# Performance work log

Hardware: AMD Instinct MI355X
Metric: run time of the kernel (lower is better)

The kernel has to match this reference:

```python
import jax, jax.numpy as jnp
import numpy as np

S, B, SC = 2048, 1024, 256 * 16  # shops, bundles, styles*colors


def setup_inputs() -> dict:
    key = jax.random.key(0)
    k1, k2, k3, k4 = jax.random.split(key, 4)
    return {
        "proba": jax.random.normal(k1, (S * B,), dtype=jnp.float32),
        "cur_inven": jax.random.uniform(k2, (S, SC), dtype=jnp.float32),
        "bun_sc": jax.random.uniform(k3, (B, SC), dtype=jnp.float32),
        "avail_bundle": jax.random.uniform(k4, (B,), dtype=jnp.float32),
        "alloc_bundle": jnp.zeros((B,), dtype=jnp.float32),
    }


def reference(proba, cur_inven, bun_sc, avail_bundle, alloc_bundle):
    # proba[i] with i = shop*B + bundle  ->  [S, B]
    p = proba.reshape(S, B)
    # constraint_multiplier: 0.01 if over-availability (p>0) or over-negative-alloc (p<0)
    over_avail = (avail_bundle[None, :] - p < 0.0) & (p > 0.0)
    over_alloc = (alloc_bundle[None, :] + p < 0.0) & (p < 0.0)
    cm = jnp.where(over_avail | over_alloc, jnp.float32(0.01), jnp.float32(1.0))
    # next_inven[s, sc] = cur[s, sc] + sum_b bun_sc[b, sc] * p[s, b] * cm[s, b]
    next_inven = cur_inven + jnp.einsum('sb,bc->sc', p * cm, bun_sc)
    return next_inven.reshape(1, -1)
```

## Files before the change

kernel.cpp:

```cpp
#include <hip/hip_runtime.h>

#define S_DIM  2048
#define B_DIM  1024
#define SC_DIM 4096

#define BM 128
#define BN 128
#define BK 64

typedef __bf16 bf16x8 __attribute__((ext_vector_type(8)));
typedef float  f32x4  __attribute__((ext_vector_type(4)));
typedef unsigned short u16x4 __attribute__((ext_vector_type(4)));
typedef unsigned short u16x8 __attribute__((ext_vector_type(8)));

__device__ __forceinline__ unsigned short f2bf(float f) {
    unsigned int u = __builtin_bit_cast(unsigned int, f);
    return (unsigned short)((u + 0x7FFFu + ((u >> 16) & 1u)) >> 16);
}

__device__ __forceinline__ void gld_lds16(const void* g, void* l) {
    __builtin_amdgcn_global_load_lds(
        (const __attribute__((address_space(1))) unsigned int*)g,
        (__attribute__((address_space(3))) unsigned int*)l, 16, 0, 0);
}

__global__ __launch_bounds__(256)
void prepack_ab(const float* __restrict__ proba,
                const float* __restrict__ avail,
                const float* __restrict__ alloc,
                const float* __restrict__ bsc,
                unsigned short* __restrict__ wsA,
                unsigned short* __restrict__ wsB)
{
    __shared__ float lds[64][129];
    const int t = threadIdx.x;

    if (blockIdx.x < 1024) {
        int c = blockIdx.x * 256 + t;
        int n = c >> 7;
        int G = c & 127;
        int k = G * 8;

        f32x4 p0 = *(const f32x4*)&proba[(size_t)n * B_DIM + k];
        f32x4 p1 = *(const f32x4*)&proba[(size_t)n * B_DIM + k + 4];
        f32x4 av0 = *(const f32x4*)&avail[k];
        f32x4 av1 = *(const f32x4*)&avail[k + 4];
        f32x4 al0 = *(const f32x4*)&alloc[k];
        f32x4 al1 = *(const f32x4*)&alloc[k + 4];

        u16x8 w;
        #pragma unroll
        for (int i = 0; i < 4; ++i) {
            float pv = p0[i];
            bool oa = (av0[i] - pv < 0.f) && (pv > 0.f);
            bool ob = (al0[i] + pv < 0.f) && (pv < 0.f);
            w[i] = f2bf(pv * ((oa || ob) ? 0.01f : 1.0f));
        }
        #pragma unroll
        for (int i = 0; i < 4; ++i) {
            float pv = p1[i];
            bool oa = (av1[i] - pv < 0.f) && (pv > 0.f);
            bool ob = (al1[i] + pv < 0.f) && (pv < 0.f);
            w[4 + i] = f2bf(pv * ((oa || ob) ? 0.01f : 1.0f));
        }
        int Gs = (G & ~7) | ((G & 7) ^ (n & 7));
        *(u16x8*)&wsA[(size_t)n * B_DIM + Gs * 8] = w;
    } else {
        int b2 = blockIdx.x - 1024;
        const int bn0 = (b2 & 31) * 128;
        const int k0  = (b2 >> 5) * 64;

        #pragma unroll
        for (int p = 0; p < 8; ++p) {
            int kl = (t >> 5) + p * 8;
            int cl = (t & 31) * 4;
            f32x4 v = *(const f32x4*)&bsc[(size_t)(k0 + kl) * SC_DIM + bn0 + cl];
            lds[kl][cl]     = v[0];
            lds[kl][cl + 1] = v[1];
            lds[kl][cl + 2] = v[2];
            lds[kl][cl + 3] = v[3];
        }
        __syncthreads();

        #pragma unroll
        for (int p = 0; p < 4; ++p) {
            int g = t & 7;
            int n = (t >> 3) + p * 32;
            u16x8 w;
            #pragma unroll
            for (int i = 0; i < 8; ++i)
                w[i] = f2bf(lds[g * 8 + i][n]);
            int gs = g ^ (n & 7);
            *(u16x8*)&wsB[(size_t)(bn0 + n) * B_DIM + k0 + gs * 8] = w;
        }
    }
}

__global__ __launch_bounds__(256, 2)
void gemm_pk(const unsigned short* __restrict__ wsA,
             const unsigned short* __restrict__ wsB,
             const float* __restrict__ cur,
             float* __restrict__ out)
{
    __shared__ __align__(16) unsigned short sA[BM * BK];
    __shared__ __align__(16) unsigned short sB[BN * BK];

    const int tid  = threadIdx.x;
    const int lane = tid & 63;
    const int wid  = tid >> 6;
    const int wm   = wid >> 1;
    const int wn   = wid & 1;
    const int l16  = lane & 15;
    const int lg   = lane >> 4;

    const int bid    = blockIdx.x;
    const int x      = bid & 7;
    const int l      = bid >> 3;
    const int n_tile = x * 4 + (l & 3);
    const int m_tile = l >> 2;
    const int bm0    = m_tile * BM;
    const int bn0    = n_tile * BN;

    const int crow = tid >> 3;
    const int cg   = tid & 7;

    f32x4 acc[4][4];
    #pragma unroll
    for (int i = 0; i < 4; ++i)
        #pragma unroll
        for (int j = 0; j < 4; ++j)
            acc[i][j] = {0.f, 0.f, 0.f, 0.f};

    auto stage = [&](int k0) {
        #pragma unroll
        for (int is = 0; is < 4; ++is)
            gld_lds16(wsA + (size_t)(bm0 + is * 32 + crow) * B_DIM + k0 + cg * 8,
                      &sA[(is * 256 + tid) * 8]);
        #pragma unroll
        for (int is = 0; is < 4; ++is)
            gld_lds16(wsB + (size_t)(bn0 + is * 32 + crow) * B_DIM + k0 + cg * 8,
                      &sB[(is * 256 + tid) * 8]);
    };

    const int NT = B_DIM / BK;
    stage(0);

    for (int t = 0; t < NT; ++t) {
        __syncthreads();

        bf16x8 afr[2][4], bfr[2][4];
        #pragma unroll
        for (int kk = 0; kk < 2; ++kk) {
            #pragma unroll
            for (int mf = 0; mf < 4; ++mf) {
                int r = wm * 64 + mf * 16 + l16;
                afr[kk][mf] = *(const bf16x8*)&sA[r * BK + (((kk * 4 + lg) ^ (r & 7)) * 8)];
            }
            #pragma unroll
            for (int nf = 0; nf < 4; ++nf) {
                int r = wn * 64 + nf * 16 + l16;
                bfr[kk][nf] = *(const bf16x8*)&sB[r * BK + (((kk * 4 + lg) ^ (r & 7)) * 8)];
            }
        }
        __syncthreads();

        if (t < NT - 1)
            stage((t + 1) * BK);
        __builtin_amdgcn_sched_barrier(0);

        #pragma unroll
        for (int kk = 0; kk < 2; ++kk)
            #pragma unroll
            for (int mf = 0; mf < 4; ++mf)
                #pragma unroll
                for (int nf = 0; nf < 4; ++nf)
                    acc[mf][nf] = __builtin_amdgcn_mfma_f32_16x16x32_bf16(
                        afr[kk][mf], bfr[kk][nf], acc[mf][nf], 0, 0, 0);
    }

    #pragma unroll
    for (int mf = 0; mf < 4; ++mf)
        #pragma unroll
        for (int j = 0; j < 4; ++j)
            #pragma unroll
            for (int nf = 0; nf < 4; ++nf) {
                int row = bm0 + wm * 64 + mf * 16 + lg * 4 + j;
                int col = bn0 + wn * 64 + nf * 16 + l16;
                size_t idx = (size_t)row * SC_DIM + col;
                out[idx] = cur[idx] + acc[mf][nf][j];
            }
}

#define FBM 128
#define FBN 128
#define LDK 72
__global__ __launch_bounds__(256, 2)
void opt_gemm_fused(const float* __restrict__ proba,
                    const float* __restrict__ cur,
                    const float* __restrict__ bsc,
                    const float* __restrict__ avail,
                    const float* __restrict__ alloc,
                    float* __restrict__ out)
{
    __shared__ __align__(16) unsigned short sA[FBM * LDK];
    __shared__ __align__(16) unsigned short sB[FBN * LDK];
    const int tid = threadIdx.x;
    const int lane = tid & 63;
    const int wid = tid >> 6;
    const int wm = wid >> 1, wn = wid & 1;
    const int bm0 = blockIdx.y * FBM, bn0 = blockIdx.x * FBN;
    const int af4 = tid & 15, ar0 = tid >> 4;
    const int bnn = tid & 127, bkh = tid >> 7;
    const int l16 = lane & 15, lg = lane >> 4;

    f32x4 acc[4][4];
    #pragma unroll
    for (int i = 0; i < 4; ++i)
        #pragma unroll
        for (int j = 0; j < 4; ++j) acc[i][j] = {0.f, 0.f, 0.f, 0.f};

    for (int k0 = 0; k0 < B_DIM; k0 += BK) {
        f32x4 av = *(const f32x4*)&avail[k0 + af4 * 4];
        f32x4 al = *(const f32x4*)&alloc[k0 + af4 * 4];
        #pragma unroll
        for (int pass = 0; pass < 8; ++pass) {
            int r = ar0 + pass * 16;
            f32x4 p = *(const f32x4*)&proba[(size_t)(bm0 + r) * B_DIM + k0 + af4 * 4];
            u16x4 w;
            #pragma unroll
            for (int i = 0; i < 4; ++i) {
                float pv = p[i];
                bool oa = (av[i] - pv < 0.f) && (pv > 0.f);
                bool ob = (al[i] + pv < 0.f) && (pv < 0.f);
                w[i] = f2bf(pv * ((oa || ob) ? 0.01f : 1.0f));
            }
            *(u16x4*)&sA[r * LDK + af4 * 4] = w;
        }
        #pragma unroll
        for (int g = 0; g < 4; ++g) {
            u16x8 w;
            #pragma unroll
            for (int i = 0; i < 8; ++i) {
                int kk = bkh * 32 + g * 8 + i;
                w[i] = f2bf(bsc[(size_t)(k0 + kk) * SC_DIM + bn0 + bnn]);
            }
            *(u16x8*)&sB[bnn * LDK + bkh * 32 + g * 8] = w;
        }
        __syncthreads();
        #pragma unroll
        for (int kk = 0; kk < 2; ++kk) {
            bf16x8 afr[4], bfr[4];
            #pragma unroll
            for (int mf = 0; mf < 4; ++mf)
                afr[mf] = *(const bf16x8*)&sA[(wm * 64 + mf * 16 + l16) * LDK + kk * 32 + lg * 8];
            #pragma unroll
            for (int nf = 0; nf < 4; ++nf)
                bfr[nf] = *(const bf16x8*)&sB[(wn * 64 + nf * 16 + l16) * LDK + kk * 32 + lg * 8];
            #pragma unroll
            for (int mf = 0; mf < 4; ++mf)
                #pragma unroll
                for (int nf = 0; nf < 4; ++nf)
                    acc[mf][nf] = __builtin_amdgcn_mfma_f32_16x16x32_bf16(
                        afr[mf], bfr[nf], acc[mf][nf], 0, 0, 0);
        }
        __syncthreads();
    }
    #pragma unroll
    for (int mf = 0; mf < 4; ++mf)
        #pragma unroll
        for (int j = 0; j < 4; ++j) {
            int row = bm0 + wm * 64 + mf * 16 + lg * 4 + j;
            #pragma unroll
            for (int nf = 0; nf < 4; ++nf) {
                int col = bn0 + wn * 64 + nf * 16 + l16;
                size_t idx = (size_t)row * SC_DIM + col;
                out[idx] = cur[idx] + acc[mf][nf][j];
            }
        }
}

extern "C" void kernel_launch(void* const* d_in, const int* in_sizes, int n_in,
                              void* d_out, int out_size, void* d_ws, size_t ws_size,
                              hipStream_t stream) {
    const float* proba = (const float*)d_in[0];
    const float* cur   = (const float*)d_in[1];
    const float* bsc   = (const float*)d_in[2];
    const float* avail = (const float*)d_in[3];
    const float* alloc = (const float*)d_in[4];
    float* out = (float*)d_out;

    const size_t wsA_bytes = (size_t)S_DIM * B_DIM * 2;
    const size_t wsB_bytes = (size_t)SC_DIM * B_DIM * 2;

    if (ws_size >= wsA_bytes + wsB_bytes) {
        unsigned short* wsA = (unsigned short*)d_ws;
        unsigned short* wsB = (unsigned short*)((char*)d_ws + wsA_bytes);

        prepack_ab<<<dim3(1024 + 512), 256, 0, stream>>>(proba, avail, alloc, bsc, wsA, wsB);
        gemm_pk<<<dim3((S_DIM / BM) * (SC_DIM / BN)), 256, 0, stream>>>(wsA, wsB, cur, out);
    } else {
        opt_gemm_fused<<<dim3(SC_DIM / FBN, S_DIM / FBM), 256, 0, stream>>>(
            proba, cur, bsc, avail, alloc, out);
    }
}
```

Before: 36.25 us.

## Prepack A in MFMA fragment order and load it directly into registers

The prepack kernel now writes the masked bf16 A operand in per-lane MFMA fragment order, so the GEMM loads A fragments straight from global memory into registers and no longer stages A through LDS. A is register double-buffered across iterations (aP/aQ) with prefetch of the next tile, while B still goes through LDS. This removes LDS traffic and shared memory for A, at the cost of more registers and uncached global loads per wave, since A rows are reread by each wn wave.

```diff
diff --git a/kernel.cpp b/kernel.cpp
--- a/kernel.cpp
+++ b/kernel.cpp
@@ -37,12 +37,17 @@
 
     if (blockIdx.x < 1024) {
         int c = blockIdx.x * 256 + t;
-        int n = c >> 7;
-        int G = c & 127;
-        int k = G * 8;
-
-        f32x4 p0 = *(const f32x4*)&proba[(size_t)n * B_DIM + k];
-        f32x4 p1 = *(const f32x4*)&proba[(size_t)n * B_DIM + k + 4];
+        int lane = c & 63;
+        int fragslot = c >> 6;
+        int mg = fragslot >> 5;
+        int kb = fragslot & 31;
+        int l16 = lane & 15;
+        int lg  = lane >> 4;
+        int row = mg * 16 + l16;
+        int k   = kb * 32 + lg * 8;
+
+        f32x4 p0 = *(const f32x4*)&proba[(size_t)row * B_DIM + k];
+        f32x4 p1 = *(const f32x4*)&proba[(size_t)row * B_DIM + k + 4];
         f32x4 av0 = *(const f32x4*)&avail[k];
         f32x4 av1 = *(const f32x4*)&avail[k + 4];
         f32x4 al0 = *(const f32x4*)&alloc[k];
@@ -63,8 +68,7 @@
             bool ob = (al1[i] + pv < 0.f) && (pv < 0.f);
             w[4 + i] = f2bf(pv * ((oa || ob) ? 0.01f : 1.0f));
         }
-        int Gs = (G & ~7) | ((G & 7) ^ (n & 7));
-        *(u16x8*)&wsA[(size_t)n * B_DIM + Gs * 8] = w;
+        *(u16x8*)&wsA[(size_t)c * 8] = w;
     } else {
         int b2 = blockIdx.x - 1024;
         const int bn0 = (b2 & 31) * 128;
@@ -102,7 +106,6 @@
              const float* __restrict__ cur,
              float* __restrict__ out)
 {
-    __shared__ __align__(16) unsigned short sA[BM * BK];
     __shared__ __align__(16) unsigned short sB[BN * BK];
 
     const int tid  = threadIdx.x;
@@ -124,6 +127,8 @@
     const int crow = tid >> 3;
     const int cg   = tid & 7;
 
+    const int mgBase = (bm0 >> 4) + wm * 4;
+
     f32x4 acc[4][4];
     #pragma unroll
     for (int i = 0; i < 4; ++i)
@@ -131,41 +136,45 @@
         for (int j = 0; j < 4; ++j)
             acc[i][j] = {0.f, 0.f, 0.f, 0.f};
 
-    auto stage = [&](int k0) {
-        #pragma unroll
-        for (int is = 0; is < 4; ++is)
-            gld_lds16(wsA + (size_t)(bm0 + is * 32 + crow) * B_DIM + k0 + cg * 8,
-                      &sA[(is * 256 + tid) * 8]);
+    auto stageB = [&](int k0) {
         #pragma unroll
         for (int is = 0; is < 4; ++is)
             gld_lds16(wsB + (size_t)(bn0 + is * 32 + crow) * B_DIM + k0 + cg * 8,
                       &sB[(is * 256 + tid) * 8]);
     };
 
-    const int NT = B_DIM / BK;
-    stage(0);
-
-    for (int t = 0; t < NT; ++t) {
-        __syncthreads();
-
-        bf16x8 afr[2][4], bfr[2][4];
-        #pragma unroll
-        for (int kk = 0; kk < 2; ++kk) {
-            #pragma unroll
-            for (int mf = 0; mf < 4; ++mf) {
-                int r = wm * 64 + mf * 16 + l16;
-                afr[kk][mf] = *(const bf16x8*)&sA[r * BK + (((kk * 4 + lg) ^ (r & 7)) * 8)];
-            }
+    const unsigned short* aBase = wsA + ((size_t)mgBase * 32 * 64 + lane) * 8;
+
+    auto loadA = [&](int t, bf16x8 (&dst)[2][4]) {
+        #pragma unroll
+        for (int kk = 0; kk < 2; ++kk)
+            #pragma unroll
+            for (int mf = 0; mf < 4; ++mf)
+                dst[kk][mf] = *(const bf16x8*)(aBase + ((size_t)(mf * 32 + 2 * t + kk)) * 512);
+    };
+
+    bf16x8 aP[2][4], aQ[2][4];
+
+    stageB(0);
+    loadA(0, aP);
+
+    auto body = [&](int t, bf16x8 (&acur)[2][4], bf16x8 (&anxt)[2][4]) {
+        __syncthreads();
+
+        bf16x8 bfr[2][4];
+        #pragma unroll
+        for (int kk = 0; kk < 2; ++kk)
             #pragma unroll
             for (int nf = 0; nf < 4; ++nf) {
                 int r = wn * 64 + nf * 16 + l16;
                 bfr[kk][nf] = *(const bf16x8*)&sB[r * BK + (((kk * 4 + lg) ^ (r & 7)) * 8)];
             }
-        }
-        __syncthreads();
-
-        if (t < NT - 1)
-            stage((t + 1) * BK);
+        __syncthreads();
+
+        if (t < B_DIM / BK - 1) {
+            stageB((t + 1) * BK);
+            loadA(t + 1, anxt);
+        }
         __builtin_amdgcn_sched_barrier(0);
 
         #pragma unroll
@@ -175,7 +184,12 @@
                 #pragma unroll
                 for (int nf = 0; nf < 4; ++nf)
                     acc[mf][nf] = __builtin_amdgcn_mfma_f32_16x16x32_bf16(
-                        afr[kk][mf], bfr[kk][nf], acc[mf][nf], 0, 0, 0);
+                        acur[kk][mf], bfr[kk][nf], acc[mf][nf], 0, 0, 0);
+    };
+
+    for (int tt = 0; tt < B_DIM / BK / 2; ++tt) {
+        body(2 * tt,     aP, aQ);
+        body(2 * tt + 1, aQ, aP);
     }
 
     #pragma unroll
```

Result: slower. 39.55 us (+9.1%).
